# Performance work log

Measured on AMD Instinct MI355X. Metric: run time of the kernel, lower is better.

The kernel has to match this reference:

```python
import jax, jax.numpy as jnp
import numpy as np

T, B, D = 1024, 64, 256   # time, batch, input dim
L, DC = 1024, 256         # context length, context dim
H, A = 256, 256           # hidden, attention dim
NEG = -1e9


def setup_inputs() -> dict:
    key = jax.random.key(0)
    ks = jax.random.split(key, 12)
    s = lambda fan: 1.0 / np.sqrt(fan)
    inp = {
        'x': jax.random.normal(ks[0], (T, B, D), jnp.float32),
        'lengths': jnp.maximum(jax.random.randint(ks[1], (B,), 1, T + 1), 1).astype(jnp.int32),
        'context': jax.random.normal(ks[2], (B, L, DC), jnp.float32),
        'ctx_lengths': jnp.maximum(jax.random.randint(ks[3], (B,), 1, L + 1), 1).astype(jnp.int32),
        'Wc': jax.random.normal(ks[4], (DC, A), jnp.float32) * s(DC),
        'Wx': jax.random.normal(ks[5], (D, A), jnp.float32) * s(D),
        'Wh': jax.random.normal(ks[6], (H, A), jnp.float32) * s(H),
        'v': jax.random.normal(ks[7], (A,), jnp.float32) * s(A),
        'W_ih': jax.random.normal(ks[8], (D + DC, 3 * H), jnp.float32) * s(D + DC),
        'W_hh': jax.random.normal(ks[9], (H, 3 * H), jnp.float32) * s(H),
        'b_ih': jnp.zeros((3 * H,), jnp.float32),
        'b_hh': jnp.zeros((3 * H,), jnp.float32),
    }
    return inp


def reference(x, lengths, context, ctx_lengths, Wc, Wx, Wh, v, W_ih, W_hh, b_ih, b_hh):
    # Precompute context projection once (shared across all timesteps). [B, L, A]
    ctx_proj = jnp.einsum('bld,da->bla', context, Wc)
    ctx_mask = jnp.arange(L)[None, :] < ctx_lengths[:, None]  # [B, L]
    h0 = jnp.zeros((B, H), x.dtype)

    def step(h, inputs):
        xt, t = inputs  # xt: [B, D]
        # Additive attention over the context.
        e = jnp.tanh(ctx_proj + (xt @ Wx)[:, None, :] + (h @ Wh)[:, None, :])  # [B, L, A]
        scores = jnp.where(ctx_mask, jnp.einsum('bla,a->bl', e, v), NEG)
        alpha = jax.nn.softmax(scores, axis=-1)                  # [B, L]
        c = jnp.einsum('bl,bld->bd', alpha, context)             # [B, DC]
        # GRU over [x_t ; c_t].
        z = jnp.concatenate([xt, c], axis=-1)                    # [B, D+DC]
        gi = z @ W_ih + b_ih
        gh = h @ W_hh + b_hh
        r = jax.nn.sigmoid(gi[:, :H] + gh[:, :H])
        u = jax.nn.sigmoid(gi[:, H:2 * H] + gh[:, H:2 * H])
        n = jnp.tanh(gi[:, 2 * H:] + r * gh[:, 2 * H:])
        h_new = u * h + (1.0 - u) * n
        valid = (t < lengths)[:, None]                           # ragged masking
        h_next = jnp.where(valid, h_new, h)
        out = jnp.where(valid, h_new, 0.0)
        return h_next, out

    h_final, outputs = jax.lax.scan(step, h0, (x, jnp.arange(T)))
    return outputs, h_final[None]  # [T, B, H], [num_layers=1, B, H]
```

## Files before the change

### kernel.cpp

```cpp
#include <hip/hip_runtime.h>
#include <cstddef>

#define T_ 1024
#define B_ 64
#define D_ 256
#define L_ 1024
#define DC_ 256
#define H_ 256
#define A_ 256
#define G3 768
#define LQ 256
#define NBLK 4

typedef unsigned int uint2v __attribute__((ext_vector_type(2)));
typedef float float4v __attribute__((ext_vector_type(4)));
typedef float float2v __attribute__((ext_vector_type(2)));

__device__ __forceinline__ float bflo(unsigned int w) { return __uint_as_float(w << 16); }
__device__ __forceinline__ float bfhi(unsigned int w) { return __uint_as_float(w & 0xffff0000u); }
__device__ __forceinline__ unsigned short f2bf(float f) {
  unsigned int x = __float_as_uint(f);
  return (unsigned short)((x + 0x7fffu + ((x >> 16) & 1u)) >> 16);
}
__device__ __forceinline__ float fast_tanh(float xx) {
  float e = __expf(2.0f * xx);
  return 1.0f - 2.0f / (e + 1.0f);
}
__device__ __forceinline__ float sigmoidf_(float xx) {
  return 1.0f / (1.0f + __expf(-xx));
}
__device__ __forceinline__ void st_agent_f(float* p, float v) {
  __hip_atomic_store(p, v, __ATOMIC_RELAXED, __HIP_MEMORY_SCOPE_AGENT);
}
__device__ __forceinline__ float ld_agent_f(const float* p) {
  return __hip_atomic_load(p, __ATOMIC_RELAXED, __HIP_MEMORY_SCOPE_AGENT);
}
__device__ __forceinline__ void group_sync(unsigned int* ctrb, unsigned int target) {
  __syncthreads();
  if (threadIdx.x == 0) {
    __hip_atomic_fetch_add(ctrb, 1u, __ATOMIC_RELEASE, __HIP_MEMORY_SCOPE_AGENT);
    while (__hip_atomic_load(ctrb, __ATOMIC_ACQUIRE, __HIP_MEMORY_SCOPE_AGENT) < target) {
      __builtin_amdgcn_s_sleep(2);
    }
  }
  __syncthreads();
}

__global__ void f2bf_kernel(const float* __restrict__ src,
                            unsigned short* __restrict__ dst, int n) {
  int i = (blockIdx.x * blockDim.x + threadIdx.x) * 4;
  if (i < n) {
    float4 v = *(const float4*)(src + i);
    ushort4 o;
    o.x = f2bf(v.x); o.y = f2bf(v.y); o.z = f2bf(v.z); o.w = f2bf(v.w);
    *(ushort4*)(dst + i) = o;
  }
}

__global__ void pack_wih_kernel(const float* __restrict__ W_ih,
                                unsigned short* __restrict__ dst) {
  int idx = blockIdx.x * 256 + threadIdx.x;
  int kb = idx / (512 * 192);
  int rem = idx % (512 * 192);
  int r = rem / 192, jg = rem % 192;
  int g = jg >> 6, jj = jg & 63;
  int j = g * 256 + kb * 64 + jj;
  dst[idx] = f2bf(W_ih[(size_t)r * G3 + j]);
}
__global__ void pack_whh_kernel(const float* __restrict__ W_hh,
                                unsigned short* __restrict__ dst) {
  int idx = blockIdx.x * 256 + threadIdx.x;
  int kb = idx / (256 * 192);
  int rem = idx % (256 * 192);
  int r = rem / 192, jg = rem % 192;
  int g = jg >> 6, jj = jg & 63;
  int j = g * 256 + kb * 64 + jj;
  dst[idx] = f2bf(W_hh[(size_t)r * G3 + j]);
}

__global__ void ctx_proj_kernel(const float* __restrict__ context,
                                const float* __restrict__ Wc,
                                unsigned short* __restrict__ ctxT) {
  __shared__ float cs[4352];
  const int bid = blockIdx.x;
  const int b = bid >> 6;
  const int l0 = (bid & 63) << 4;
  const int tid = threadIdx.x;
  for (int idx = tid; idx < 16 * DC_; idx += 256) {
    int r = idx >> 8;
    int d = idx & 255;
    cs[r * DC_ + d] = context[((size_t)b * L_ + (l0 + r)) * DC_ + d];
  }
  __syncthreads();
  const int a = tid;
  float acc[16];
#pragma unroll
  for (int r = 0; r < 16; ++r) acc[r] = 0.0f;
  for (int d = 0; d < DC_; ++d) {
    float w = Wc[d * A_ + a];
#pragma unroll
    for (int r = 0; r < 16; ++r) acc[r] += cs[r * DC_ + d] * w;
  }
  __syncthreads();
#pragma unroll
  for (int r = 0; r < 16; ++r) cs[a * 17 + r] = acc[r];
  __syncthreads();
  for (int idx = tid; idx < 16 * A_; idx += 256) {
    int aa = idx >> 4;
    int r = idx & 15;
    ctxT[((size_t)b * A_ + aa) * L_ + l0 + r] = f2bf(cs[aa * 17 + r]);
  }
}

__global__ __launch_bounds__(1024) void encoder_kernel(
    const float* __restrict__ x, const int* __restrict__ lengths,
    const float* __restrict__ context, const int* __restrict__ ctx_lengths,
    const unsigned short* __restrict__ wx_b, const unsigned short* __restrict__ wh_b,
    const float* __restrict__ v,
    const unsigned short* __restrict__ wih_pk, const unsigned short* __restrict__ whh_pk,
    const float* __restrict__ b_ih, const float* __restrict__ b_hh,
    const unsigned short* __restrict__ ctxT, float* __restrict__ out,
    float* __restrict__ cpart, float* __restrict__ hx, unsigned int* __restrict__ ctr) {
  __shared__ __align__(16) unsigned short ctx_lds[A_ * LQ];
  __shared__ __align__(16) float scratch[4096];
  __shared__ __align__(16) float xt_s[D_];
  __shared__ __align__(16) float h_s[H_];
  __shared__ __align__(16) float c_s[DC_];
  __shared__ float2 qv_s[A_];
  __shared__ float pv_s[LQ];
  __shared__ float gatI[192], gatH[192];
  __shared__ float bsl_i[192], bsl_h[192];
  __shared__ float wsum_l[4];

  const int gb = blockIdx.x;
  const int b = gb >> 2, kb = gb & 3;
  const int tid = threadIdx.x;
  const int len = lengths[b];
  const int clen = ctx_lengths[b];
  const int lbase = kb * LQ;
  const unsigned short* ctxTb = ctxT + (size_t)b * A_ * L_;
  const float* ctxb = context + (size_t)b * L_ * DC_;
  const unsigned short* wihp = wih_pk + (size_t)kb * (512 * 192);
  const unsigned short* whhp = whh_pk + (size_t)kb * (256 * 192);
  float* cpart_grp = cpart + (size_t)b * NBLK * 264;
  float* cpart_my = cpart_grp + kb * 264;
  float* hx_b = hx + (size_t)b * 256;
  unsigned int* ctr_b = ctr + b * 32;

  const int p16 = tid >> 6, i64 = tid & 63;

  if (tid < 256) { h_s[tid] = 0.0f; qv_s[tid] = make_float2(0.0f, v[tid]); }
  if (tid < 192) {
    int g = tid >> 6, jj = tid & 63;
    int j = g * 256 + kb * 64 + jj;
    bsl_i[tid] = b_ih[j]; bsl_h[tid] = b_hh[j];
  }
  for (int idx = tid; idx < 16384; idx += 1024) {
    int a = idx >> 6;
    int lq = idx & 63;
    *(uint2v*)&ctx_lds[a * LQ + lq * 4] =
        *(const uint2v*)(ctxTb + (size_t)a * L_ + lbase + lq * 4);
  }
  __syncthreads();

  for (int t = 0; t < len; ++t) {
    if (tid < 64) {
      *(float4v*)&xt_s[tid * 4] =
          *(const float4v*)&x[((size_t)t * B_ + b) * D_ + tid * 4];
    }
    __syncthreads();

    {
      const int a0 = i64 * 4, k0 = p16 * 16;
      float4v acc = {0.f, 0.f, 0.f, 0.f};
#pragma unroll
      for (int k = k0; k < k0 + 16; ++k) {
        float xv = xt_s[k];
        uint2v w = *(const uint2v*)(wx_b + (size_t)k * A_ + a0);
        acc.x += xv * bflo(w.x); acc.y += xv * bfhi(w.x);
        acc.z += xv * bflo(w.y); acc.w += xv * bfhi(w.y);
      }
#pragma unroll
      for (int k = k0; k < k0 + 16; ++k) {
        float hv = h_s[k];
        uint2v w = *(const uint2v*)(wh_b + (size_t)k * A_ + a0);
        acc.x += hv * bflo(w.x); acc.y += hv * bfhi(w.x);
        acc.z += hv * bflo(w.y); acc.w += hv * bfhi(w.y);
      }
      *(float4v*)&scratch[tid * 4] = acc;
    }
    __syncthreads();
    if (tid < 256) {
      float q = 0.f;
#pragma unroll
      for (int p = 0; p < 16; ++p) q += scratch[p * 256 + tid];
      qv_s[tid].x = q;
    }
    __syncthreads();

    {
      const int ll0 = i64 * 4;
      float4v acc = {0.f, 0.f, 0.f, 0.f};
      if (lbase + ll0 < clen) {
        const unsigned short* basep = ctx_lds + p16 * 16 * LQ + ll0;
#pragma unroll 4
        for (int aa = 0; aa < 16; ++aa) {
          uint2v w = *(const uint2v*)(basep + aa * LQ);
          float2 qv = qv_s[p16 * 16 + aa];
          acc.x += qv.y * fast_tanh(bflo(w.x) + qv.x);
          acc.y += qv.y * fast_tanh(bfhi(w.x) + qv.x);
          acc.z += qv.y * fast_tanh(bflo(w.y) + qv.x);
          acc.w += qv.y * fast_tanh(bfhi(w.y) + qv.x);
        }
      }
      *(float4v*)&scratch[tid * 4] = acc;
    }
    __syncthreads();
    if (tid < 256) {
      float s = 0.f;
#pragma unroll
      for (int p = 0; p < 16; ++p) s += scratch[p * 256 + tid];
      int lg = lbase + tid;
      float e = (lg < clen) ? __expf(s) : 0.f;
      pv_s[tid] = e;
      float sm = e;
#pragma unroll
      for (int off = 32; off; off >>= 1) sm += __shfl_xor(sm, off);
      if ((tid & 63) == 0) wsum_l[tid >> 6] = sm;
    }
    __syncthreads();

    {
      const int d0 = i64 * 4;
      const int lmax = min(LQ, max(0, clen - lbase));
      const int l0 = p16 * 16, l1 = min(l0 + 16, lmax);
      float4v acc = {0.f, 0.f, 0.f, 0.f};
      for (int l = l0; l < l1; ++l) {
        float pv = pv_s[l];
        float4v cv = *(const float4v*)&ctxb[(size_t)(lbase + l) * DC_ + d0];
        acc.x += pv * cv.x; acc.y += pv * cv.y; acc.z += pv * cv.z; acc.w += pv * cv.w;
      }
      *(float4v*)&scratch[tid * 4] = acc;
    }
    __syncthreads();
    if (tid < 256) {
      float cp = 0.f;
#pragma unroll
      for (int p = 0; p < 16; ++p) cp += scratch[p * 256 + tid];
      st_agent_f(&cpart_my[tid], cp);
    }
    if (tid == 0) {
      st_agent_f(&cpart_my[256], wsum_l[0] + wsum_l[1] + wsum_l[2] + wsum_l[3]);
    }
    group_sync(ctr_b, 8u * t + 4u);
    if (tid < 256) {
      float cc = 0.f, ss = 0.f;
#pragma unroll
      for (int k2 = 0; k2 < 4; ++k2) {
        cc += ld_agent_f(cpart_grp + k2 * 264 + tid);
        ss += ld_agent_f(cpart_grp + k2 * 264 + 256);
      }
      c_s[tid] = cc / ss;
    }
    __syncthreads();

    if (tid < 768) {
      const int pq = tid / 96;
      const int jc = tid % 96;
      const float* zsrc = (pq < 4) ? xt_s : c_s;
      const int zoff = (pq < 4) ? pq * 64 : (pq - 4) * 64;
      const int r0 = pq * 64;
      float a0 = 0.f, a1 = 0.f;
#pragma unroll 8
      for (int i = 0; i < 64; ++i) {
        float zk = zsrc[zoff + i];
        unsigned int w = *(const unsigned int*)(wihp + (size_t)(r0 + i) * 192 + 2 * jc);
        a0 += zk * bflo(w); a1 += zk * bfhi(w);
      }
      const int rh0 = pq * 32;
      float h0 = 0.f, h1 = 0.f;
#pragma unroll 8
      for (int i = 0; i < 32; ++i) {
        float hv = h_s[rh0 + i];
        unsigned int w = *(const unsigned int*)(whhp + (size_t)(rh0 + i) * 192 + 2 * jc);
        h0 += hv * bflo(w); h1 += hv * bfhi(w);
      }
      *(float2v*)&scratch[pq * 192 + 2 * jc] = float2v{a0, a1};
      *(float2v*)&scratch[1536 + pq * 192 + 2 * jc] = float2v{h0, h1};
    }
    __syncthreads();
    if (tid < 192) {
      float gi = bsl_i[tid], gh = bsl_h[tid];
#pragma unroll
      for (int p = 0; p < 8; ++p) {
        gi += scratch[p * 192 + tid];
        gh += scratch[1536 + p * 192 + tid];
      }
      gatI[tid] = gi; gatH[tid] = gh;
    }
    __syncthreads();
    if (tid < 64) {
      float r = sigmoidf_(gatI[tid] + gatH[tid]);
      float u = sigmoidf_(gatI[64 + tid] + gatH[64 + tid]);
      float n = fast_tanh(gatI[128 + tid] + r * gatH[128 + tid]);
      float hn = u * h_s[kb * 64 + tid] + (1.0f - u) * n;
      st_agent_f(&hx_b[kb * 64 + tid], hn);
      __builtin_nontemporal_store(hn, &out[((size_t)t * B_ + b) * H_ + kb * 64 + tid]);
    }
    group_sync(ctr_b, 8u * t + 8u);
    if (tid < 256) h_s[tid] = ld_agent_f(&hx_b[tid]);
    __syncthreads();
  }

  {
    const int n = (T_ - len) * 64;
    for (int idx = tid; idx < n; idx += 1024) {
      int tt = len + (idx >> 6);
      int ii = idx & 63;
      __builtin_nontemporal_store(0.0f, &out[((size_t)tt * B_ + b) * H_ + kb * 64 + ii]);
    }
  }
  if (tid < 64) {
    out[(size_t)T_ * B_ * H_ + (size_t)b * H_ + kb * 64 + tid] = h_s[kb * 64 + tid];
  }
}

extern "C" void kernel_launch(void* const* d_in, const int* in_sizes, int n_in,
                              void* d_out, int out_size, void* d_ws, size_t ws_size,
                              hipStream_t stream) {
  const float* x = (const float*)d_in[0];
  const int* lengths = (const int*)d_in[1];
  const float* context = (const float*)d_in[2];
  const int* ctx_lengths = (const int*)d_in[3];
  const float* Wc = (const float*)d_in[4];
  const float* Wx = (const float*)d_in[5];
  const float* Wh = (const float*)d_in[6];
  const float* v = (const float*)d_in[7];
  const float* W_ih = (const float*)d_in[8];
  const float* W_hh = (const float*)d_in[9];
  const float* b_ih = (const float*)d_in[10];
  const float* b_hh = (const float*)d_in[11];
  float* out = (float*)d_out;

  char* w = (char*)d_ws;
  unsigned short* ctxT = (unsigned short*)w;
  unsigned short* wx_b = (unsigned short*)(w + 33554432);
  unsigned short* wh_b = (unsigned short*)(w + 33685504);
  unsigned short* wih_pk = (unsigned short*)(w + 33816576);
  unsigned short* whh_pk = (unsigned short*)(w + 34603008);
  float* cpart = (float*)(w + 34996224);
  float* hx = (float*)(w + 35266560);
  unsigned int* ctr = (unsigned int*)(w + 35332096);

  hipMemsetAsync(ctr, 0, 8192, stream);
  hipLaunchKernelGGL(f2bf_kernel, dim3(64), dim3(256), 0, stream, Wx, wx_b, D_ * A_);
  hipLaunchKernelGGL(f2bf_kernel, dim3(64), dim3(256), 0, stream, Wh, wh_b, H_ * A_);
  hipLaunchKernelGGL(pack_wih_kernel, dim3(1536), dim3(256), 0, stream, W_ih, wih_pk);
  hipLaunchKernelGGL(pack_whh_kernel, dim3(768), dim3(256), 0, stream, W_hh, whh_pk);
  hipLaunchKernelGGL(ctx_proj_kernel, dim3(B_ * (L_ / 16)), dim3(256), 0, stream,
                     context, Wc, ctxT);
  hipLaunchKernelGGL(encoder_kernel, dim3(B_ * NBLK), dim3(1024), 0, stream,
                     x, lengths, context, ctx_lengths, wx_b, wh_b, v,
                     wih_pk, whh_pk, b_ih, b_hh, ctxT, out, cpart, hx, ctr);
}
```

Baseline: 56.16 ms.

## Split group barrier to overlap GRU x/h matvecs, cache context in registers

```diff
diff --git a/kernel.cpp b/kernel.cpp
--- a/kernel.cpp
+++ b/kernel.cpp
@@ -22,6 +22,9 @@
   unsigned int x = __float_as_uint(f);
   return (unsigned short)((x + 0x7fffu + ((x >> 16) & 1u)) >> 16);
 }
+__device__ __forceinline__ unsigned int packbf(float lo, float hi) {
+  return (unsigned int)f2bf(lo) | ((unsigned int)f2bf(hi) << 16);
+}
 __device__ __forceinline__ float fast_tanh(float xx) {
   float e = __expf(2.0f * xx);
   return 1.0f - 2.0f / (e + 1.0f);
@@ -35,11 +38,15 @@
 __device__ __forceinline__ float ld_agent_f(const float* p) {
   return __hip_atomic_load(p, __ATOMIC_RELAXED, __HIP_MEMORY_SCOPE_AGENT);
 }
-__device__ __forceinline__ void group_sync(unsigned int* ctrb, unsigned int target) {
+__device__ __forceinline__ void group_arrive(unsigned int* ctrb) {
   __syncthreads();
   if (threadIdx.x == 0) {
     __hip_atomic_fetch_add(ctrb, 1u, __ATOMIC_RELEASE, __HIP_MEMORY_SCOPE_AGENT);
-    while (__hip_atomic_load(ctrb, __ATOMIC_ACQUIRE, __HIP_MEMORY_SCOPE_AGENT) < target) {
+  }
+}
+__device__ __forceinline__ void group_wait(unsigned int* ctrb, unsigned int target) {
+  if (threadIdx.x == 0) {
+    while (__hip_atomic_load(ctrb, __ATOMIC_RELAXED, __HIP_MEMORY_SCOPE_AGENT) < target) {
       __builtin_amdgcn_s_sleep(2);
     }
   }
@@ -133,7 +140,7 @@
   __shared__ float wsum_l[4];
 
   const int gb = blockIdx.x;
-  const int b = gb >> 2, kb = gb & 3;
+  const int b = gb & 63, kb = gb >> 6;
   const int tid = threadIdx.x;
   const int len = lengths[b];
   const int clen = ctx_lengths[b];
@@ -148,6 +155,7 @@
   unsigned int* ctr_b = ctr + b * 32;
 
   const int p16 = tid >> 6, i64 = tid & 63;
+  const int pq = tid / 96, jc = tid % 96;
 
   if (tid < 256) { h_s[tid] = 0.0f; qv_s[tid] = make_float2(0.0f, v[tid]); }
   if (tid < 192) {
@@ -160,6 +168,13 @@
     int lq = idx & 63;
     *(uint2v*)&ctx_lds[a * LQ + lq * 4] =
         *(const uint2v*)(ctxTb + (size_t)a * L_ + lbase + lq * 4);
+  }
+  uint2v creg[16];
+#pragma unroll
+  for (int i = 0; i < 16; ++i) {
+    float4v cv = *(const float4v*)&ctxb[(size_t)(lbase + p16 * 16 + i) * DC_ + i64 * 4];
+    creg[i].x = packbf(cv.x, cv.y);
+    creg[i].y = packbf(cv.z, cv.w);
   }
   __syncthreads();
 
@@ -231,14 +246,13 @@
     __syncthreads();
 
     {
-      const int d0 = i64 * 4;
-      const int lmax = min(LQ, max(0, clen - lbase));
-      const int l0 = p16 * 16, l1 = min(l0 + 16, lmax);
       float4v acc = {0.f, 0.f, 0.f, 0.f};
-      for (int l = l0; l < l1; ++l) {
-        float pv = pv_s[l];
-        float4v cv = *(const float4v*)&ctxb[(size_t)(lbase + l) * DC_ + d0];
-        acc.x += pv * cv.x; acc.y += pv * cv.y; acc.z += pv * cv.z; acc.w += pv * cv.w;
+#pragma unroll
+      for (int i = 0; i < 16; ++i) {
+        float pv = pv_s[p16 * 16 + i];
+        uint2v w = creg[i];
+        acc.x += pv * bflo(w.x); acc.y += pv * bfhi(w.x);
+        acc.z += pv * bflo(w.y); acc.w += pv * bfhi(w.y);
       }
       *(float4v*)&scratch[tid * 4] = acc;
     }
@@ -252,38 +266,19 @@
     if (tid == 0) {
       st_agent_f(&cpart_my[256], wsum_l[0] + wsum_l[1] + wsum_l[2] + wsum_l[3]);
     }
-    group_sync(ctr_b, 8u * t + 4u);
-    if (tid < 256) {
-      float cc = 0.f, ss = 0.f;
-#pragma unroll
-      for (int k2 = 0; k2 < 4; ++k2) {
-        cc += ld_agent_f(cpart_grp + k2 * 264 + tid);
-        ss += ld_agent_f(cpart_grp + k2 * 264 + 256);
-      }
-      c_s[tid] = cc / ss;
-    }
-    __syncthreads();
+    group_arrive(ctr_b);
 
     if (tid < 768) {
-      const int pq = tid / 96;
-      const int jc = tid % 96;
-      const float* zsrc = (pq < 4) ? xt_s : c_s;
-      const int zoff = (pq < 4) ? pq * 64 : (pq - 4) * 64;
-      const int r0 = pq * 64;
-      float a0 = 0.f, a1 = 0.f;
-#pragma unroll 8
-      for (int i = 0; i < 64; ++i) {
-        float zk = zsrc[zoff + i];
-        unsigned int w = *(const unsigned int*)(wihp + (size_t)(r0 + i) * 192 + 2 * jc);
-        a0 += zk * bflo(w); a1 += zk * bfhi(w);
-      }
-      const int rh0 = pq * 32;
-      float h0 = 0.f, h1 = 0.f;
+      const int r0 = pq * 32;
+      float a0 = 0.f, a1 = 0.f, h0 = 0.f, h1 = 0.f;
 #pragma unroll 8
       for (int i = 0; i < 32; ++i) {
-        float hv = h_s[rh0 + i];
-        unsigned int w = *(const unsigned int*)(whhp + (size_t)(rh0 + i) * 192 + 2 * jc);
-        h0 += hv * bflo(w); h1 += hv * bfhi(w);
+        float zk = xt_s[r0 + i];
+        unsigned int wi = *(const unsigned int*)(wihp + (size_t)(r0 + i) * 192 + 2 * jc);
+        a0 += zk * bflo(wi); a1 += zk * bfhi(wi);
+        float hv = h_s[r0 + i];
+        unsigned int wh = *(const unsigned int*)(whhp + (size_t)(r0 + i) * 192 + 2 * jc);
+        h0 += hv * bflo(wh); h1 += hv * bfhi(wh);
       }
       *(float2v*)&scratch[pq * 192 + 2 * jc] = float2v{a0, a1};
       *(float2v*)&scratch[1536 + pq * 192 + 2 * jc] = float2v{h0, h1};
@@ -297,6 +292,42 @@
         gh += scratch[1536 + p * 192 + tid];
       }
       gatI[tid] = gi; gatH[tid] = gh;
+    }
+    group_wait(ctr_b, 8u * t + 4u);
+
+    {
+      float cc = 0.f;
+      if (tid < 256) {
+#pragma unroll
+        for (int k2 = 0; k2 < 4; ++k2) cc += ld_agent_f(cpart_grp + k2 * 264 + tid);
+      } else if (tid < 260) {
+        wsum_l[tid - 256] = ld_agent_f(cpart_grp + (tid - 256) * 264 + 256);
+      }
+      __syncthreads();
+      if (tid < 256) {
+        c_s[tid] = cc / (wsum_l[0] + wsum_l[1] + wsum_l[2] + wsum_l[3]);
+      }
+    }
+    __syncthreads();
+
+    if (tid < 768) {
+      const int r0 = pq * 32;
+      float b0 = 0.f, b1 = 0.f;
+#pragma unroll 8
+      for (int i = 0; i < 32; ++i) {
+        float zk = c_s[r0 + i];
+        unsigned int wi =
+            *(const unsigned int*)(wihp + (size_t)(256 + r0 + i) * 192 + 2 * jc);
+        b0 += zk * bflo(wi); b1 += zk * bfhi(wi);
+      }
+      *(float2v*)&scratch[pq * 192 + 2 * jc] = float2v{b0, b1};
+    }
+    __syncthreads();
+    if (tid < 192) {
+      float gi = gatI[tid];
+#pragma unroll
+      for (int p = 0; p < 8; ++p) gi += scratch[p * 192 + tid];
+      gatI[tid] = gi;
     }
     __syncthreads();
     if (tid < 64) {
@@ -307,7 +338,8 @@
       st_agent_f(&hx_b[kb * 64 + tid], hn);
       __builtin_nontemporal_store(hn, &out[((size_t)t * B_ + b) * H_ + kb * 64 + tid]);
     }
-    group_sync(ctr_b, 8u * t + 8u);
+    group_arrive(ctr_b);
+    group_wait(ctr_b, 8u * t + 8u);
     if (tid < 256) h_s[tid] = ld_agent_f(&hx_b[tid]);
     __syncthreads();
   }
```

Result: slower. 58.41 ms (+4.0%).
